# Kernel tuning notes

Hardware: AMD Instinct MI355X
Metric: run time of the kernel (lower is better)

The kernel has to match this reference:

```python
import jax, jax.numpy as jnp
import numpy as np

N = 50000    # nodes
E = 800000   # edges (avg degree 16)
DIN = 128    # input_dim
DH = 32      # hidden_dim (per-head channels)
H = 4        # heads


def setup_inputs() -> dict:
    key = jax.random.key(0)
    ks = jax.random.split(key, 32)
    inp = {}
    inp["x"] = jax.random.normal(ks[0], (N, DIN), dtype=jnp.float32)
    inp["edge_index"] = jax.random.randint(ks[1], (2, E), 0, N)
    # layer dims: (in, qkv_out, skip_out). Layers 0,1 concat heads (H*DH); layer 2 averages (DH).
    dims = [(DIN, H * DH, H * DH), (H * DH, H * DH, H * DH), (H * DH, H * DH, DH)]
    ki = 2
    for li, (din, dqkv, dskip) in enumerate(dims):
        for nm, do in (("q", dqkv), ("k", dqkv), ("v", dqkv), ("s", dskip)):
            inp[f"W{nm}{li}"] = jax.random.normal(ks[ki], (din, do), dtype=jnp.float32) * (1.0 / np.sqrt(din))
            ki += 1
            inp[f"b{nm}{li}"] = jax.random.normal(ks[ki], (do,), dtype=jnp.float32) * 0.01
            ki += 1
    return inp


def _transformer_conv(x, src, dst, Wq, bq, Wk, bk, Wv, bv, Ws, bs, concat):
    # PyG TransformerConv (beta=False, root_weight=True, eval mode -> no attn dropout)
    n = x.shape[0]
    q = (x @ Wq + bq).reshape(n, -1, DH)  # [N,H,d]
    k = (x @ Wk + bk).reshape(n, -1, DH)
    v = (x @ Wv + bv).reshape(n, -1, DH)
    # per-edge attention logits: q_i . k_j / sqrt(d), i=dst, j=src
    logits = jnp.einsum('ehd,ehd->eh', q[dst], k[src]) * (1.0 / np.sqrt(DH))  # [E,H]
    m = jax.ops.segment_max(logits, dst, num_segments=n)          # scatter-softmax max
    a = jnp.exp(logits - m[dst])
    s = jax.ops.segment_sum(a, dst, num_segments=n)
    alpha = a / s[dst]                                            # [E,H]
    msg = v[src] * alpha[..., None]                               # [E,H,d]
    agg = jax.ops.segment_sum(msg.reshape(msg.shape[0], -1), dst, num_segments=n)
    agg = agg.reshape(n, -1, DH)
    out = agg.reshape(n, -1) if concat else agg.mean(axis=1)
    return out + x @ Ws + bs  # root/skip connection


def reference(x, edge_index,
              Wq0, bq0, Wk0, bk0, Wv0, bv0, Ws0, bs0,
              Wq1, bq1, Wk1, bk1, Wv1, bv1, Ws1, bs1,
              Wq2, bq2, Wk2, bk2, Wv2, bv2, Ws2, bs2):
    src, dst = edge_index[0], edge_index[1]
    h = _transformer_conv(x, src, dst, Wq0, bq0, Wk0, bk0, Wv0, bv0, Ws0, bs0, True)
    h = jax.nn.relu(h)  # dropout is identity in eval
    h = _transformer_conv(h, src, dst, Wq1, bq1, Wk1, bk1, Wv1, bv1, Ws1, bs1, True)
    h = jax.nn.relu(h)
    out = _transformer_conv(h, src, dst, Wq2, bq2, Wk2, bk2, Wv2, bv2, Ws2, bs2, False)
    return out  # [N, DH]
```

## Files before the change

kernel.cpp:

```cpp
#include <hip/hip_runtime.h>
#include <cstdint>
#include <cstddef>

#define DIN 128
#define ROW_BYTES 1280

typedef __attribute__((ext_vector_type(8))) short short8v;
typedef __attribute__((ext_vector_type(4))) float float4v;

__global__ void k_zero(int* __restrict__ a, int n){
  int i = blockIdx.x*blockDim.x + threadIdx.x;
  if(i<n) a[i]=0;
}

__global__ void k_count(const int* __restrict__ dst, int* __restrict__ deg, int E){
  int i = blockIdx.x*blockDim.x + threadIdx.x;
  if(i<E) atomicAdd(&deg[dst[i]], 1);
}

__global__ void k_scan1(const int* __restrict__ deg, int* __restrict__ offs,
                        int* __restrict__ part, int n){
  __shared__ int sm[256];
  int t = threadIdx.x; int g = blockIdx.x*256 + t;
  int v = (g<n)? deg[g] : 0;
  sm[t] = v;
  for(int o=1;o<256;o<<=1){
    __syncthreads();
    int x = (t>=o)? sm[t-o] : 0;
    __syncthreads();
    sm[t] += x;
  }
  __syncthreads();
  if(g<n) offs[g+1] = sm[t];
  if(t==255) part[blockIdx.x] = sm[255];
}

__global__ void k_scan2(int* __restrict__ part, int nb){
  __shared__ int sm[256];
  int t=threadIdx.x;
  int v = (t<nb)? part[t] : 0;
  sm[t]=v;
  for(int o=1;o<256;o<<=1){ __syncthreads(); int x=(t>=o)?sm[t-o]:0; __syncthreads(); sm[t]+=x; }
  __syncthreads();
  if(t<nb) part[t] = sm[t]-v;
}

__global__ void k_scan3(int* __restrict__ offs, const int* __restrict__ part, int n){
  int t=threadIdx.x; int g=blockIdx.x*256+t;
  if(g<n) offs[g+1] += part[blockIdx.x];
  if(g==0) offs[0]=0;
}

__global__ void k_scatter(const int* __restrict__ src, const int* __restrict__ dst,
                          const int* __restrict__ offs, int* __restrict__ cur,
                          int* __restrict__ srcs, int E){
  int i=blockIdx.x*blockDim.x+threadIdx.x;
  if(i<E){
    int d = dst[i];
    int p = atomicAdd(&cur[d],1);
    srcs[offs[d]+p] = src[i];
  }
}

__device__ inline unsigned f2bf(float x){
  unsigned u = __float_as_uint(x);
  return (u + 0x7FFFu + ((u>>16)&1u)) >> 16;
}
__device__ inline unsigned pack2(float a, float b){ return f2bf(a) | (f2bf(b)<<16); }
__device__ inline float bflo(unsigned w){ return __uint_as_float(w<<16); }
__device__ inline float bfhi(unsigned w){ return __uint_as_float(w & 0xFFFF0000u); }

__global__ void k_wt(
  const float* __restrict__ W0, const float* __restrict__ W1, const float* __restrict__ W2,
  const float* __restrict__ W3, const float* __restrict__ W4, const float* __restrict__ W5,
  const float* __restrict__ W6, const float* __restrict__ W7, const float* __restrict__ W8,
  const float* __restrict__ W9, const float* __restrict__ W10, const float* __restrict__ W11,
  unsigned short* __restrict__ wt)
{
  int i = blockIdx.y;
  int e = blockIdx.x*256 + threadIdx.x;
  int dout = (i==11)? 32 : 128;
  if(e >= dout*128) return;
  const float* W;
  switch(i){
    case 0: W=W0; break; case 1: W=W1; break; case 2: W=W2; break; case 3: W=W3; break;
    case 4: W=W4; break; case 5: W=W5; break; case 6: W=W6; break; case 7: W=W7; break;
    case 8: W=W8; break; case 9: W=W9; break; case 10: W=W10; break; default: W=W11; break;
  }
  int c = e % dout, k = e / dout;
  wt[i*16384 + c*128 + k] = (unsigned short)f2bf(W[(size_t)k*dout + c]);
}

__global__ __launch_bounds__(256,4) void k_gemm(
  const void* __restrict__ Xv, int xbf, int nrows,
  const unsigned short* __restrict__ Wt,
  const float* __restrict__ bq, const float* __restrict__ bk,
  const float* __restrict__ bv, const float* __restrict__ bs,
  int ws_cols, char* __restrict__ out)
{
  __shared__ unsigned short Xs[64][136];
  __shared__ unsigned short Wsh[64][136];
  int t = threadIdx.x;
  int row0 = blockIdx.x*64;
  {
    int r = t>>2, kb = (t&3)*32;
    int gr = row0 + r;
    if(gr < nrows){
      if(xbf){
        const unsigned short* xp = (const unsigned short*)Xv + (size_t)gr*DIN + kb;
        #pragma unroll
        for(int j=0;j<4;j++)
          *(uint4*)&Xs[r][kb + j*8] = *(const uint4*)(xp + j*8);
      } else {
        const float* xp = (const float*)Xv + (size_t)gr*DIN + kb;
        #pragma unroll
        for(int j=0;j<4;j++){
          float4 fa = *(const float4*)(xp + j*8);
          float4 fb = *(const float4*)(xp + j*8 + 4);
          uint4 pk = make_uint4(pack2(fa.x,fa.y), pack2(fa.z,fa.w),
                                pack2(fb.x,fb.y), pack2(fb.z,fb.w));
          *(uint4*)&Xs[r][kb + j*8] = pk;
        }
      }
    } else {
      uint4 z = make_uint4(0,0,0,0);
      #pragma unroll
      for(int j=0;j<4;j++) *(uint4*)&Xs[r][kb + j*8] = z;
    }
  }
  int wv = t>>6, l = t&63;
  int lr = l & 15, lk = (l>>4)*8;
  for(int mat=0; mat<4; mat++){
    int wcols = (mat==3)? ws_cols : 128;
    const unsigned short* Wm = Wt + mat*16384;
    const float* bias = (mat==0)?bq:(mat==1)?bk:(mat==2)?bv:bs;
    for(int half=0; half<2; half++){
      int col0 = half*64;
      if(col0 >= wcols) break;
      {
        int c = t>>2, kb = (t&3)*32;
        int gc = col0 + c;
        if(gc < wcols){
          const unsigned short* wp = Wm + (size_t)gc*128 + kb;
          #pragma unroll
          for(int j=0;j<4;j++)
            *(uint4*)&Wsh[c][kb + j*8] = *(const uint4*)(wp + j*8);
        } else {
          uint4 z = make_uint4(0,0,0,0);
          #pragma unroll
          for(int j=0;j<4;j++) *(uint4*)&Wsh[c][kb + j*8] = z;
        }
      }
      __syncthreads();
      float4v acc[4];
      #pragma unroll
      for(int mt=0;mt<4;mt++) acc[mt] = (float4v){0.f,0.f,0.f,0.f};
      #pragma unroll
      for(int kk=0;kk<4;kk++){
        short8v b = *(const short8v*)&Wsh[wv*16 + lr][kk*32 + lk];
        #pragma unroll
        for(int mt=0;mt<4;mt++){
          short8v a = *(const short8v*)&Xs[mt*16 + lr][kk*32 + lk];
          acc[mt] = __builtin_amdgcn_mfma_f32_16x16x32_bf16(a, b, acc[mt], 0, 0, 0);
        }
      }
      int col = col0 + wv*16 + lr;
      bool cok = col < wcols;
      float bcol = cok ? bias[col] : 0.f;
      int rb = row0 + (l>>4)*4;
      #pragma unroll
      for(int mt=0;mt<4;mt++){
        #pragma unroll
        for(int j=0;j<4;j++){
          int r = rb + mt*16 + j;
          if(r < nrows && cok){
            float val = acc[mt][j] + bcol;
            char* rowp = out + (size_t)r*ROW_BYTES;
            if(mat==0)      *(unsigned short*)(rowp + col*2) = (unsigned short)f2bf(val);
            else if(mat==3) *(float*)(rowp + 768 + col*4) = val;
            else {
              int h = col>>5, d = col&31;
              int off = ((mat==1)?256:512) + (d>>3)*64 + h*16 + (d&7)*2;
              *(unsigned short*)(rowp + off) = (unsigned short)f2bf(val);
            }
          }
        }
      }
      __syncthreads();
    }
  }
}

__global__ __launch_bounds__(256,4) void k_attn(
  const char* __restrict__ QKVS, const int* __restrict__ offs,
  const int* __restrict__ srcs, void* __restrict__ outv, int mode, int n)
{
  int wv = threadIdx.x>>6, lane = threadIdx.x&63;
  int node = blockIdx.x*4 + wv;
  if(node >= n) return;
  int h = lane & 3;
  int e_l = lane >> 2;
  const float rs = 0.17677669529663687f;
  const char* rowq = QKVS + (size_t)node*ROW_BYTES + h*64;
  float4 q[8];
  #pragma unroll
  for(int j=0;j<4;j++){
    uint4 qw = *(const uint4*)(rowq + j*16);
    q[2*j]   = make_float4(bflo(qw.x)*rs, bfhi(qw.x)*rs, bflo(qw.y)*rs, bfhi(qw.y)*rs);
    q[2*j+1] = make_float4(bflo(qw.z)*rs, bfhi(qw.z)*rs, bflo(qw.w)*rs, bfhi(qw.w)*rs);
  }
  int beg = offs[node], end = offs[node+1];
  float m = -__builtin_inff(), s = 0.f;
  float4 acc[8];
  #pragma unroll
  for(int j=0;j<8;j++) acc[j] = make_float4(0.f,0.f,0.f,0.f);

  for(int b0 = beg; b0 < end; b0 += 16){
    int idx = b0 + e_l;
    bool valid = idx < end;
    int sj = srcs[valid ? idx : beg];
    const char* base = QKVS + (size_t)sj*ROW_BYTES + 256 + h*16;
    uint4 vw[4];
    #pragma unroll
    for(int j=0;j<4;j++) vw[j] = *(const uint4*)(base + 256 + j*64);
    #pragma unroll
    for(int j=0;j<4;j++)
      asm volatile("" : "+v"(vw[j].x), "+v"(vw[j].y), "+v"(vw[j].z), "+v"(vw[j].w));
    float dot = 0.f;
    #pragma unroll
    for(int j=0;j<4;j++){
      uint4 kw = *(const uint4*)(base + j*64);
      float4 qa = q[2*j], qb = q[2*j+1];
      dot += qa.x*bflo(kw.x) + qa.y*bfhi(kw.x) + qa.z*bflo(kw.y) + qa.w*bfhi(kw.y);
      dot += qb.x*bflo(kw.z) + qb.y*bfhi(kw.z) + qb.z*bflo(kw.w) + qb.w*bfhi(kw.w);
    }
    float logit = valid ? dot : -__builtin_inff();
    float bm = logit;
    bm = fmaxf(bm, __shfl_xor(bm,4));
    bm = fmaxf(bm, __shfl_xor(bm,8));
    bm = fmaxf(bm, __shfl_xor(bm,16));
    bm = fmaxf(bm, __shfl_xor(bm,32));
    float mn = fmaxf(m, bm);
    float r = __expf(m - mn);
    float p = __expf(logit - mn);
    float ps = p;
    ps += __shfl_xor(ps,4); ps += __shfl_xor(ps,8); ps += __shfl_xor(ps,16); ps += __shfl_xor(ps,32);
    s = r*s + ps; m = mn;
    #pragma unroll
    for(int j=0;j<4;j++){
      uint4 w = vw[j];
      float4 a0 = acc[2*j], a1 = acc[2*j+1];
      a0.x = fmaf(a0.x, r, p*bflo(w.x)); a0.y = fmaf(a0.y, r, p*bfhi(w.x));
      a0.z = fmaf(a0.z, r, p*bflo(w.y)); a0.w = fmaf(a0.w, r, p*bfhi(w.y));
      a1.x = fmaf(a1.x, r, p*bflo(w.z)); a1.y = fmaf(a1.y, r, p*bfhi(w.z));
      a1.z = fmaf(a1.z, r, p*bflo(w.w)); a1.w = fmaf(a1.w, r, p*bfhi(w.w));
      acc[2*j] = a0; acc[2*j+1] = a1;
    }
  }
  int b5 = (lane>>5)&1, b4 = (lane>>4)&1, b3 = (lane>>3)&1, b2 = (lane>>2)&1;
  float4 r4[4];
  #pragma unroll
  for(int j=0;j<4;j++){
    float4 keep = b5 ? acc[j+4] : acc[j];
    float4 send = b5 ? acc[j]   : acc[j+4];
    keep.x += __shfl_xor(send.x,32); keep.y += __shfl_xor(send.y,32);
    keep.z += __shfl_xor(send.z,32); keep.w += __shfl_xor(send.w,32);
    r4[j] = keep;
  }
  float4 r2[2];
  #pragma unroll
  for(int j=0;j<2;j++){
    float4 keep = b4 ? r4[j+2] : r4[j];
    float4 send = b4 ? r4[j]   : r4[j+2];
    keep.x += __shfl_xor(send.x,16); keep.y += __shfl_xor(send.y,16);
    keep.z += __shfl_xor(send.z,16); keep.w += __shfl_xor(send.w,16);
    r2[j] = keep;
  }
  float4 r1;
  {
    float4 keep = b3 ? r2[1] : r2[0];
    float4 send = b3 ? r2[0] : r2[1];
    keep.x += __shfl_xor(send.x,8); keep.y += __shfl_xor(send.y,8);
    keep.z += __shfl_xor(send.z,8); keep.w += __shfl_xor(send.w,8);
    r1 = keep;
  }
  float fx, fy;
  {
    float kx = b2 ? r1.z : r1.x, ky = b2 ? r1.w : r1.y;
    float sx = b2 ? r1.x : r1.z, sy = b2 ? r1.y : r1.w;
    fx = kx + __shfl_xor(sx,4);
    fy = ky + __shfl_xor(sy,4);
  }
  float inv = (s > 0.f) ? (1.f/s) : 0.f;
  if(mode == 0){
    const float* sk = (const float*)(QKVS + (size_t)node*ROW_BYTES + 768);
    float2 sv = *(const float2*)(sk + h*32 + 2*e_l);
    float ox = fmaxf(fmaf(fx, inv, sv.x), 0.f);
    float oy = fmaxf(fmaf(fy, inv, sv.y), 0.f);
    ((unsigned*)outv)[(size_t)node*64 + h*16 + e_l] = pack2(ox, oy);
  } else {
    float sc = inv*0.25f;
    float ox = fx*sc, oy = fy*sc;
    ox += __shfl_xor(ox,1); oy += __shfl_xor(oy,1);
    ox += __shfl_xor(ox,2); oy += __shfl_xor(oy,2);
    if(h == 0){
      const float* sk = (const float*)(QKVS + (size_t)node*ROW_BYTES + 768);
      float2 sv = *(const float2*)(sk + 2*e_l);
      float* op = (float*)outv + (size_t)node*32 + 2*e_l;
      op[0] = ox + sv.x; op[1] = oy + sv.y;
    }
  }
}

extern "C" void kernel_launch(void* const* d_in, const int* in_sizes, int n_in,
                              void* d_out, int out_size, void* d_ws, size_t ws_size,
                              hipStream_t stream) {
  const float* x = (const float*)d_in[0];
  const int* ei = (const int*)d_in[1];
  int n = in_sizes[0]/DIN;
  int E = in_sizes[1]/2;
  const int* esrc = ei;
  const int* edst = ei + E;

  char* w = (char*)d_ws;
  auto alloc = [&](size_t bytes)->char*{
    char* p = w; w += (bytes + 255) & ~(size_t)255; return p;
  };
  int* offs = (int*)alloc((size_t)(n+1)*4);
  int* deg  = (int*)alloc((size_t)n*4);
  int* cur  = (int*)alloc((size_t)n*4);
  int* part = (int*)alloc(256*4);
  int* srcs = (int*)alloc((size_t)E*4);
  char* qkvs = alloc((size_t)n*ROW_BYTES);
  unsigned short* h1 = (unsigned short*)alloc((size_t)n*128*2);
  unsigned short* h2 = (unsigned short*)alloc((size_t)n*128*2);
  unsigned short* wt = (unsigned short*)alloc((size_t)12*16384*2);

  auto f = [&](int i)->const float*{ return (const float*)d_in[i]; };

  hipLaunchKernelGGL(k_wt, dim3(64,12), dim3(256), 0, stream,
                     f(2),f(4),f(6),f(8), f(10),f(12),f(14),f(16), f(18),f(20),f(22),f(24), wt);

  int SB = (n+255)/256;
  hipLaunchKernelGGL(k_zero, dim3((n+255)/256), dim3(256), 0, stream, deg, n);
  hipLaunchKernelGGL(k_zero, dim3((n+255)/256), dim3(256), 0, stream, cur, n);
  hipLaunchKernelGGL(k_count, dim3((E+255)/256), dim3(256), 0, stream, edst, deg, E);
  hipLaunchKernelGGL(k_scan1, dim3(SB), dim3(256), 0, stream, deg, offs, part, n);
  hipLaunchKernelGGL(k_scan2, dim3(1), dim3(256), 0, stream, part, SB);
  hipLaunchKernelGGL(k_scan3, dim3(SB), dim3(256), 0, stream, offs, part, n);
  hipLaunchKernelGGL(k_scatter, dim3((E+255)/256), dim3(256), 0, stream, esrc, edst, offs, cur, srcs, E);

  int RT = (n+63)/64;
  int AB = (n+3)/4;

  hipLaunchKernelGGL(k_gemm, dim3(RT), dim3(256), 0, stream,
                     (const void*)x, 0, n, wt + 0*4*16384, f(3),f(5),f(7),f(9), 128, qkvs);
  hipLaunchKernelGGL(k_attn, dim3(AB), dim3(256), 0, stream, qkvs, offs, srcs, (void*)h1, 0, n);
  hipLaunchKernelGGL(k_gemm, dim3(RT), dim3(256), 0, stream,
                     (const void*)h1, 1, n, wt + 1*4*16384, f(11),f(13),f(15),f(17), 128, qkvs);
  hipLaunchKernelGGL(k_attn, dim3(AB), dim3(256), 0, stream, qkvs, offs, srcs, (void*)h2, 0, n);
  hipLaunchKernelGGL(k_gemm, dim3(RT), dim3(256), 0, stream,
                     (const void*)h2, 1, n, wt + 2*4*16384, f(19),f(21),f(23),f(25), 32, qkvs);
  hipLaunchKernelGGL(k_attn, dim3(AB), dim3(256), 0, stream, qkvs, offs, srcs, d_out, 1, n);
}
```

Measured before the change: 464.6 us.

## Shrink QKVS rows to 1 KB with bf16 skip, double-buffer K gathers in attention

```diff
diff --git a/kernel.cpp b/kernel.cpp
--- a/kernel.cpp
+++ b/kernel.cpp
@@ -3,15 +3,10 @@
 #include <cstddef>
 
 #define DIN 128
-#define ROW_BYTES 1280
+#define ROW_BYTES 1024
 
 typedef __attribute__((ext_vector_type(8))) short short8v;
 typedef __attribute__((ext_vector_type(4))) float float4v;
-
-__global__ void k_zero(int* __restrict__ a, int n){
-  int i = blockIdx.x*blockDim.x + threadIdx.x;
-  if(i<n) a[i]=0;
-}
 
 __global__ void k_count(const int* __restrict__ dst, int* __restrict__ deg, int E){
   int i = blockIdx.x*blockDim.x + threadIdx.x;
@@ -175,9 +170,9 @@
           int r = rb + mt*16 + j;
           if(r < nrows && cok){
             float val = acc[mt][j] + bcol;
-            char* rowp = out + (size_t)r*ROW_BYTES;
+            char* rowp = out + ((size_t)r<<10);
             if(mat==0)      *(unsigned short*)(rowp + col*2) = (unsigned short)f2bf(val);
-            else if(mat==3) *(float*)(rowp + 768 + col*4) = val;
+            else if(mat==3) *(unsigned short*)(rowp + 768 + col*2) = (unsigned short)f2bf(val);
             else {
               int h = col>>5, d = col&31;
               int off = ((mat==1)?256:512) + (d>>3)*64 + h*16 + (d&7)*2;
@@ -201,60 +196,96 @@
   int h = lane & 3;
   int e_l = lane >> 2;
   const float rs = 0.17677669529663687f;
-  const char* rowq = QKVS + (size_t)node*ROW_BYTES + h*64;
-  float4 q[8];
+  const char* rowq = QKVS + ((size_t)node<<10) + h*64;
+  uint4 qw[4];
   #pragma unroll
-  for(int j=0;j<4;j++){
-    uint4 qw = *(const uint4*)(rowq + j*16);
-    q[2*j]   = make_float4(bflo(qw.x)*rs, bfhi(qw.x)*rs, bflo(qw.y)*rs, bfhi(qw.y)*rs);
-    q[2*j+1] = make_float4(bflo(qw.z)*rs, bfhi(qw.z)*rs, bflo(qw.w)*rs, bfhi(qw.w)*rs);
-  }
+  for(int j=0;j<4;j++) qw[j] = *(const uint4*)(rowq + j*16);
   int beg = offs[node], end = offs[node+1];
-  float m = -__builtin_inff(), s = 0.f;
+  float m = 0.f, s = 0.f;
   float4 acc[8];
   #pragma unroll
   for(int j=0;j<8;j++) acc[j] = make_float4(0.f,0.f,0.f,0.f);
 
-  for(int b0 = beg; b0 < end; b0 += 16){
-    int idx = b0 + e_l;
-    bool valid = idx < end;
-    int sj = srcs[valid ? idx : beg];
-    const char* base = QKVS + (size_t)sj*ROW_BYTES + 256 + h*16;
-    uint4 vw[4];
-    #pragma unroll
-    for(int j=0;j<4;j++) vw[j] = *(const uint4*)(base + 256 + j*64);
-    #pragma unroll
-    for(int j=0;j<4;j++)
-      asm volatile("" : "+v"(vw[j].x), "+v"(vw[j].y), "+v"(vw[j].z), "+v"(vw[j].w));
-    float dot = 0.f;
-    #pragma unroll
-    for(int j=0;j<4;j++){
-      uint4 kw = *(const uint4*)(base + j*64);
-      float4 qa = q[2*j], qb = q[2*j+1];
-      dot += qa.x*bflo(kw.x) + qa.y*bfhi(kw.x) + qa.z*bflo(kw.y) + qa.w*bfhi(kw.y);
-      dot += qb.x*bflo(kw.z) + qb.y*bfhi(kw.z) + qb.z*bflo(kw.w) + qb.w*bfhi(kw.w);
-    }
-    float logit = valid ? dot : -__builtin_inff();
-    float bm = logit;
-    bm = fmaxf(bm, __shfl_xor(bm,4));
-    bm = fmaxf(bm, __shfl_xor(bm,8));
-    bm = fmaxf(bm, __shfl_xor(bm,16));
-    bm = fmaxf(bm, __shfl_xor(bm,32));
-    float mn = fmaxf(m, bm);
-    float r = __expf(m - mn);
-    float p = __expf(logit - mn);
-    float ps = p;
-    ps += __shfl_xor(ps,4); ps += __shfl_xor(ps,8); ps += __shfl_xor(ps,16); ps += __shfl_xor(ps,32);
-    s = r*s + ps; m = mn;
-    #pragma unroll
-    for(int j=0;j<4;j++){
-      uint4 w = vw[j];
-      float4 a0 = acc[2*j], a1 = acc[2*j+1];
-      a0.x = fmaf(a0.x, r, p*bflo(w.x)); a0.y = fmaf(a0.y, r, p*bfhi(w.x));
-      a0.z = fmaf(a0.z, r, p*bflo(w.y)); a0.w = fmaf(a0.w, r, p*bfhi(w.y));
-      a1.x = fmaf(a1.x, r, p*bflo(w.z)); a1.y = fmaf(a1.y, r, p*bfhi(w.z));
-      a1.z = fmaf(a1.z, r, p*bflo(w.w)); a1.w = fmaf(a1.w, r, p*bfhi(w.w));
-      acc[2*j] = a0; acc[2*j+1] = a1;
+  if(beg < end){
+    uint4 kA[4], kB[4];
+    const char* baseA = nullptr; const char* baseB = nullptr;
+    bool mA = false, mB = false;
+
+    auto issueK = [&](int b0, uint4* kw, const char** basep)->bool{
+      int idx = b0 + e_l;
+      bool msk = idx < end;
+      const char* base = QKVS + ((size_t)srcs[msk ? idx : beg]<<10) + 256 + h*16;
+      #pragma unroll
+      for(int j=0;j<4;j++) kw[j] = *(const uint4*)(base + j*64);
+      *basep = base;
+      return msk;
+    };
+
+    auto proc = [&](const uint4* kw, const char* base, bool msk, bool first){
+      uint4 vw[4];
+      #pragma unroll
+      for(int j=0;j<4;j++) vw[j] = *(const uint4*)(base + 256 + j*64);
+      float dot = 0.f;
+      #pragma unroll
+      for(int j=0;j<4;j++){
+        uint4 kwj = kw[j]; uint4 qj = qw[j];
+        dot += bflo(qj.x)*bflo(kwj.x) + bfhi(qj.x)*bfhi(kwj.x);
+        dot += bflo(qj.y)*bflo(kwj.y) + bfhi(qj.y)*bfhi(kwj.y);
+        dot += bflo(qj.z)*bflo(kwj.z) + bfhi(qj.z)*bfhi(kwj.z);
+        dot += bflo(qj.w)*bflo(kwj.w) + bfhi(qj.w)*bfhi(kwj.w);
+      }
+      dot *= rs;
+      float logit = msk ? dot : -__builtin_inff();
+      float bm = logit;
+      bm = fmaxf(bm, __shfl_xor(bm,4));
+      bm = fmaxf(bm, __shfl_xor(bm,8));
+      bm = fmaxf(bm, __shfl_xor(bm,16));
+      bm = fmaxf(bm, __shfl_xor(bm,32));
+      float mn = first ? bm : fmaxf(m, bm);
+      float p = __expf(logit - mn);
+      float ps = p;
+      ps += __shfl_xor(ps,4); ps += __shfl_xor(ps,8); ps += __shfl_xor(ps,16); ps += __shfl_xor(ps,32);
+      if(first){
+        s = ps; m = mn;
+        #pragma unroll
+        for(int j=0;j<4;j++){
+          uint4 w = vw[j];
+          acc[2*j]   = make_float4(p*bflo(w.x), p*bfhi(w.x), p*bflo(w.y), p*bfhi(w.y));
+          acc[2*j+1] = make_float4(p*bflo(w.z), p*bfhi(w.z), p*bflo(w.w), p*bfhi(w.w));
+        }
+      } else {
+        float r = __expf(m - mn);
+        s = r*s + ps; m = mn;
+        #pragma unroll
+        for(int j=0;j<4;j++){
+          uint4 w = vw[j];
+          float4 a0 = acc[2*j], a1 = acc[2*j+1];
+          a0.x = fmaf(a0.x, r, p*bflo(w.x)); a0.y = fmaf(a0.y, r, p*bfhi(w.x));
+          a0.z = fmaf(a0.z, r, p*bflo(w.y)); a0.w = fmaf(a0.w, r, p*bfhi(w.y));
+          a1.x = fmaf(a1.x, r, p*bflo(w.z)); a1.y = fmaf(a1.y, r, p*bfhi(w.z));
+          a1.z = fmaf(a1.z, r, p*bflo(w.w)); a1.w = fmaf(a1.w, r, p*bfhi(w.w));
+          acc[2*j] = a0; acc[2*j+1] = a1;
+        }
+      }
+    };
+
+    mA = issueK(beg, kA, &baseA);
+    int b1 = beg + 16;
+    if(b1 < end) mB = issueK(b1, kB, &baseB);
+    proc(kA, baseA, mA, true);
+    int bcur = b1;
+    bool useB = true;
+    while(bcur < end){
+      int nxt = bcur + 16;
+      if(useB){
+        if(nxt < end) mA = issueK(nxt, kA, &baseA);
+        proc(kB, baseB, mB, false);
+      } else {
+        if(nxt < end) mB = issueK(nxt, kB, &baseB);
+        proc(kA, baseA, mA, false);
+      }
+      useB = !useB;
+      bcur = nxt;
     }
   }
   int b5 = (lane>>5)&1, b4 = (lane>>4)&1, b3 = (lane>>3)&1, b2 = (lane>>2)&1;
@@ -293,10 +324,9 @@
   }
   float inv = (s > 0.f) ? (1.f/s) : 0.f;
   if(mode == 0){
-    const float* sk = (const float*)(QKVS + (size_t)node*ROW_BYTES + 768);
-    float2 sv = *(const float2*)(sk + h*32 + 2*e_l);
-    float ox = fmaxf(fmaf(fx, inv, sv.x), 0.f);
-    float oy = fmaxf(fmaf(fy, inv, sv.y), 0.f);
+    unsigned sw = *(const unsigned*)(QKVS + ((size_t)node<<10) + 768 + h*64 + e_l*4);
+    float ox = fmaxf(fmaf(fx, inv, bflo(sw)), 0.f);
+    float oy = fmaxf(fmaf(fy, inv, bfhi(sw)), 0.f);
     ((unsigned*)outv)[(size_t)node*64 + h*16 + e_l] = pack2(ox, oy);
   } else {
     float sc = inv*0.25f;
@@ -304,10 +334,9 @@
     ox += __shfl_xor(ox,1); oy += __shfl_xor(oy,1);
     ox += __shfl_xor(ox,2); oy += __shfl_xor(oy,2);
     if(h == 0){
-      const float* sk = (const float*)(QKVS + (size_t)node*ROW_BYTES + 768);
-      float2 sv = *(const float2*)(sk + 2*e_l);
+      unsigned sw = *(const unsigned*)(QKVS + ((size_t)node<<10) + 768 + e_l*4);
       float* op = (float*)outv + (size_t)node*32 + 2*e_l;
-      op[0] = ox + sv.x; op[1] = oy + sv.y;
+      op[0] = ox + bflo(sw); op[1] = oy + bfhi(sw);
     }
   }
 }
@@ -342,8 +371,8 @@
                      f(2),f(4),f(6),f(8), f(10),f(12),f(14),f(16), f(18),f(20),f(22),f(24), wt);
 
   int SB = (n+255)/256;
-  hipLaunchKernelGGL(k_zero, dim3((n+255)/256), dim3(256), 0, stream, deg, n);
-  hipLaunchKernelGGL(k_zero, dim3((n+255)/256), dim3(256), 0, stream, cur, n);
+  hipMemsetAsync(deg, 0, (size_t)n*4, stream);
+  hipMemsetAsync(cur, 0, (size_t)n*4, stream);
   hipLaunchKernelGGL(k_count, dim3((E+255)/256), dim3(256), 0, stream, edst, deg, E);
   hipLaunchKernelGGL(k_scan1, dim3(SB), dim3(256), 0, stream, deg, offs, part, n);
   hipLaunchKernelGGL(k_scan2, dim3(1), dim3(256), 0, stream, part, SB);
```

Result: slower. 562.3 us (+21.0%).
